# Performance work log

Hardware: AMD Instinct MI355X
Metric: run time of the kernel (lower is better)

Reference implementation:

```python
import jax, jax.numpy as jnp
import numpy as np

W_DIM = 512
NF = 128          # n_features (all blocks equal)
NB = 4            # num_layers / n_blocks
B = 8             # batch
INIT = 32         # initial resolution: 2**(8 - 4 + 1)
IMG = 256         # 2**log_resolution
EPS = 1e-8


def setup_inputs() -> dict:
    key = jax.random.key(0)
    ks = jax.random.split(key, 12)
    d = {}
    d["w"] = jax.random.normal(ks[0], (NB, B, W_DIM), jnp.float32)
    for i in range(NB):
        r = INIT * (2 ** i)
        d[f"noise{i}"] = jax.random.normal(ks[1 + i], (2, B, 1, r, r), jnp.float32)
    # learned parameters
    d["initial_constant"] = jax.random.normal(ks[5], (1, NF, INIT, INIT), jnp.float32)
    d["to_style_w"] = jax.random.normal(ks[6], (NB, NF, W_DIM), jnp.float32)      # EqualizedLinear weights
    d["to_style_b"] = 0.1 * jax.random.normal(ks[7], (NB, NF), jnp.float32)
    d["conv_w"] = jax.random.normal(ks[8], (NB, 2, NF, NF, 3, 3), jnp.float32)    # two StyleBlock convs per block
    d["scale_noise"] = 0.1 * jax.random.normal(ks[9], (NB, 2), jnp.float32)
    d["style_bias"] = 0.1 * jax.random.normal(ks[10], (NB, 2, NF), jnp.float32)
    d["rgb_w"] = jax.random.normal(ks[11], (NB, 1, NF, 1, 1), jnp.float32)        # ToRGB 1x1 convs
    return d


def _resize(x, h, w):
    # bilinear, half-pixel centers (matches F.interpolate align_corners=False)
    return jax.image.resize(x, (x.shape[0], x.shape[1], h, w), "bilinear")


def _mod_conv(x, s, weight, demodulate):
    # x: [B, Cin, H, W], s: [B, Cin], weight: [Cout, Cin, k, k]
    out_c, in_c, k, _ = weight.shape
    c = 1.0 / np.sqrt(in_c * k * k)  # EqualizedWeight scale
    ws = (weight * c)[None] * s[:, None, :, None, None]  # [B, Cout, Cin, k, k]
    if demodulate:
        ws = ws * jax.lax.rsqrt(jnp.sum(ws * ws, axis=(2, 3, 4), keepdims=True) + EPS)
    conv = lambda xi, wi: jax.lax.conv_general_dilated(xi[None], wi, (1, 1), "SAME")[0]
    return jax.vmap(conv)(x, ws)  # per-sample weights == grouped conv with groups=B


def _style_block(x, s, wconv, sn, b, noise):
    x = _mod_conv(x, s, wconv, True)
    x = x + sn * noise
    return jax.nn.leaky_relu(x + b[None, :, None, None], 0.2)


def reference(w, noise0, noise1, noise2, noise3, initial_constant, to_style_w,
              to_style_b, conv_w, scale_noise, style_bias, rgb_w):
    noises = [noise0, noise1, noise2, noise3]
    b = w.shape[1]
    x = jax.nn.relu(jnp.broadcast_to(initial_constant, (b,) + initial_constant.shape[1:]))
    cl = 1.0 / np.sqrt(W_DIM)  # EqualizedLinear scale
    rgb_sum = jnp.zeros((b, 1, IMG, IMG), x.dtype)
    for i in range(NB):
        if i > 0:
            x = _resize(x, x.shape[2] * 2, x.shape[3] * 2)
        s = w[i] @ (to_style_w[i] * cl).T + to_style_b[i]  # [B, NF]
        x = _style_block(x, s, conv_w[i, 0], scale_noise[i, 0], style_bias[i, 0], noises[i][0])
        x = _style_block(x, s, conv_w[i, 1], scale_noise[i, 1], style_bias[i, 1], noises[i][1])
        rgb = _mod_conv(x, s, rgb_w[i], False)  # [B, 1, h, w]
        rgb_sum = rgb_sum + _resize(rgb, IMG, IMG)
    return rgb_sum / 2 + 0.5
```

## Files before the change

### kernel.cpp

```cpp
#include <hip/hip_runtime.h>
#include <math.h>

#define NB 4
#define BATCH 8
#define NF 128
#define WDIM 512
#define EPS_D 1e-8f

typedef unsigned short ushortT;
typedef __attribute__((ext_vector_type(8))) short short8v;
typedef __attribute__((ext_vector_type(8))) unsigned short ushort8v;
typedef __attribute__((ext_vector_type(4))) float float4v;
typedef __attribute__((ext_vector_type(4))) unsigned int uint4v;
typedef __attribute__((ext_vector_type(2))) unsigned int uint2v;

__device__ inline unsigned short f2bf(float f) {
    unsigned u = __builtin_bit_cast(unsigned, f);
    u = (u + 0x7fffu + ((u >> 16) & 1u)) >> 16;
    return (unsigned short)u;
}
__device__ inline float bf2f(unsigned short h) {
    unsigned u = ((unsigned)h) << 16;
    return __builtin_bit_cast(float, u);
}

__global__ void k_style(const float* __restrict__ w,
                        const float* __restrict__ tsw,
                        const float* __restrict__ tsb,
                        float* __restrict__ s) {
    int gid = blockIdx.x * blockDim.x + threadIdx.x;
    if (gid >= NB * BATCH * NF) return;
    int i = gid >> 10;
    int b = (gid >> 7) & 7;
    int o = gid & 127;
    const float cl = 0.044194173824159216f;
    const float* wr = w + (i * BATCH + b) * WDIM;
    const float* tr = tsw + (i * NF + o) * WDIM;
    float acc = 0.f;
    for (int k = 0; k < WDIM; ++k) acc += wr[k] * tr[k];
    s[gid] = acc * cl + tsb[i * NF + o];
}

__global__ void k_demod(const float* __restrict__ conv_w,
                        const float* __restrict__ s,
                        float* __restrict__ d) {
    int bx = blockIdx.x;
    int l = bx >> 7;
    int o = bx & 127;
    int lane = threadIdx.x;
    const float* wb = conv_w + (size_t)((l * NF + o) * NF) * 9;
    float t0 = 0.f, t1 = 0.f;
    for (int k = 0; k < 9; ++k) {
        float a = wb[lane * 9 + k];        t0 += a * a;
        float c = wb[(lane + 64) * 9 + k]; t1 += c * c;
    }
    const float c2 = 1.0f / 1152.0f;
    int i = l >> 1;
    for (int b = 0; b < BATCH; ++b) {
        float s0 = s[(i * BATCH + b) * NF + lane];
        float s1 = s[(i * BATCH + b) * NF + lane + 64];
        float v = t0 * s0 * s0 + t1 * s1 * s1;
        for (int off = 32; off > 0; off >>= 1) v += __shfl_down(v, off);
        if (lane == 0) d[(l * BATCH + b) * NF + o] = rsqrtf(v * c2 + EPS_D);
    }
}

__global__ void k_wmodF(const float* __restrict__ cw, const float* __restrict__ s,
                        ushortT* __restrict__ wm) {
    int idx = blockIdx.x * blockDim.x + threadIdx.x;
    int lane = idx & 63;
    int mf = (idx >> 6) & 7;
    int kcc = (idx >> 9) & 3;
    int t = (idx >> 11) % 9;
    int r2 = idx / (2048 * 9);
    int b = r2 & 7;
    int l = r2 >> 3;
    if (l >= 8) return;
    const float cscale = 0.029462782549439483f;
    int co = mf * 16 + (lane & 15);
    int kb = kcc * 32 + (lane >> 4) * 8;
    const float* src = cw + (((size_t)l * NF + co) * NF) * 9;
    const float* sr = s + ((l >> 1) * BATCH + b) * NF;
    ushort8v o;
    #pragma unroll
    for (int e = 0; e < 8; ++e) {
        int ci = kb + e;
        o[e] = f2bf(src[(size_t)ci * 9 + t] * cscale * sr[ci]);
    }
    *(ushort8v*)(wm + (size_t)idx * 8) = o;
}

__global__ void k_prep_init(const float* __restrict__ ic, ushortT* __restrict__ xp,
                            int total) {
    for (int idx = blockIdx.x * blockDim.x + threadIdx.x; idx < total;
         idx += gridDim.x * blockDim.x) {
        int ci = idx & 127;
        int p = (idx >> 7) & 1023;
        float v = ic[ci * 1024 + p];
        xp[idx] = f2bf(v > 0.f ? v : 0.f);
    }
}

__global__ void k_up2_bf(const ushortT* __restrict__ in, ushortT* __restrict__ out,
                         int h, int w, int total) {
    int W2 = w * 2, H2 = h * 2;
    for (int gid = blockIdx.x * blockDim.x + threadIdx.x; gid < total;
         gid += gridDim.x * blockDim.x) {
        int cg = gid & 15;
        int t = gid >> 4;
        int ox = t % W2; t /= W2;
        int oy = t % H2; int zb = t / H2;
        int y0 = (oy >> 1) - 1 + (oy & 1);
        float wy0 = (oy & 1) ? 0.75f : 0.25f;
        int x0 = (ox >> 1) - 1 + (ox & 1);
        float wx0 = (ox & 1) ? 0.75f : 0.25f;
        int y1 = min(y0 + 1, h - 1); y0 = max(y0, 0);
        int x1 = min(x0 + 1, w - 1); x0 = max(x0, 0);
        const ushortT* base = in + (size_t)zb * h * w * 128 + cg * 8;
        ushort8v v00 = *(const ushort8v*)(base + (size_t)(y0 * w + x0) * 128);
        ushort8v v01 = *(const ushort8v*)(base + (size_t)(y0 * w + x1) * 128);
        ushort8v v10 = *(const ushort8v*)(base + (size_t)(y1 * w + x0) * 128);
        ushort8v v11 = *(const ushort8v*)(base + (size_t)(y1 * w + x1) * 128);
        float wy1 = 1.f - wy0, wx1 = 1.f - wx0;
        ushort8v o;
        #pragma unroll
        for (int k = 0; k < 8; ++k) {
            float v = wy0 * (wx0 * bf2f(v00[k]) + wx1 * bf2f(v01[k]))
                    + wy1 * (wx0 * bf2f(v10[k]) + wx1 * bf2f(v11[k]));
            o[k] = f2bf(v);
        }
        *(ushort8v*)(out + ((size_t)(zb * H2 + oy) * W2 + ox) * 128 + cg * 8) = o;
    }
}

template<int UP2, int NOY>
__global__ __launch_bounds__(256, 3) void k_conv7(
    const ushortT* __restrict__ xp, ushortT* __restrict__ yp,
    const ushortT* __restrict__ wF,
    const float* __restrict__ d_b,
    const float* __restrict__ nz,
    const float* __restrict__ bias,
    const float* __restrict__ sn_ptr,
    const float* __restrict__ s_blk,
    const float* __restrict__ rgbw_i,
    float* __restrict__ rgbb,
    int H, int W, int b0, int do_rgb)
{
    __shared__ __align__(16) char lb[46080];
    int tid = threadIdx.x;
    int lane = tid & 63;
    int wv = tid >> 6;
    int wm = wv & 1;
    int wn = wv >> 1;
    int lm = lane & 15, lk = lane >> 4;
    int tilesX = W >> 4;
    int tx0 = (blockIdx.x % tilesX) << 4;
    int ty0 = (blockIdx.x / tilesX) << 3;
    int zb = blockIdx.y;
    int b = b0 + zb;

    if (!UP2) {
        const char* xbase = (const char*)(xp + (size_t)zb * H * W * 128);
        int offs[6];
        #pragma unroll
        for (int it = 0; it < 6; ++it) {
            int cw = it * 64 + lane;
            int off = -1;
            if (cw < 360) {
                int chunk = wv * 360 + cw;
                int px = chunk >> 3, slot = chunk & 7;
                int hy = px / 18, hx = px - hy * 18;
                int gy = ty0 + hy - 1, gx = tx0 + hx - 1;
                if ((unsigned)gy < (unsigned)H && (unsigned)gx < (unsigned)W)
                    off = (gy * W + gx) * 256 + ((slot ^ (px & 7)) << 4);
            }
            offs[it] = off;
        }
        {
            const uint4v zv = {0, 0, 0, 0};
            #pragma unroll
            for (int c = 0; c < 12; ++c) {
                int idx = tid + c * 256;
                if (idx < 2880) *(uint4v*)(lb + idx * 16) = zv;
            }
        }
        __syncthreads();
        #pragma unroll
        for (int it = 0; it < 6; ++it)
            if (offs[it] >= 0)
                __builtin_amdgcn_global_load_lds(
                    (const __attribute__((address_space(1))) void*)(xbase + offs[it]),
                    (__attribute__((address_space(3))) void*)(lb + wv * 5760 + it * 1024), 16, 0, 0);
        __syncthreads();
        #pragma unroll
        for (int it = 0; it < 6; ++it)
            if (offs[it] >= 0)
                __builtin_amdgcn_global_load_lds(
                    (const __attribute__((address_space(1))) void*)(xbase + offs[it] + 128),
                    (__attribute__((address_space(3))) void*)(lb + 23040 + wv * 5760 + it * 1024), 16, 0, 0);
    } else {
        int h2 = H >> 1, w2 = W >> 1;
        const char* xbase = (const char*)(xp + (size_t)zb * h2 * w2 * 128);
        #pragma unroll
        for (int cih = 0; cih < 2; ++cih) {
            for (int it = 0; it < 6; ++it) {
                int cw = it * 64 + lane;
                if (cw >= 360) break;
                int chunk = wv * 360 + cw;
                int px = chunk >> 3, slot = chunk & 7;
                int hy = px / 18, hx = px - hy * 18;
                int gy = ty0 + hy - 1, gx = tx0 + hx - 1;
                ushort8v o = {0, 0, 0, 0, 0, 0, 0, 0};
                if ((unsigned)gy < (unsigned)H && (unsigned)gx < (unsigned)W) {
                    int sby = ((slot ^ (px & 7)) << 4) + cih * 128;
                    int y0 = (gy >> 1) - 1 + (gy & 1);
                    float wy0 = (gy & 1) ? 0.75f : 0.25f;
                    int x0 = (gx >> 1) - 1 + (gx & 1);
                    float wx0 = (gx & 1) ? 0.75f : 0.25f;
                    int y1 = min(y0 + 1, h2 - 1); y0 = max(y0, 0);
                    int x1 = min(x0 + 1, w2 - 1); x0 = max(x0, 0);
                    ushort8v v00 = *(const ushort8v*)(xbase + (y0 * w2 + x0) * 256 + sby);
                    ushort8v v01 = *(const ushort8v*)(xbase + (y0 * w2 + x1) * 256 + sby);
                    ushort8v v10 = *(const ushort8v*)(xbase + (y1 * w2 + x0) * 256 + sby);
                    ushort8v v11 = *(const ushort8v*)(xbase + (y1 * w2 + x1) * 256 + sby);
                    float wy1 = 1.f - wy0, wx1 = 1.f - wx0;
                    #pragma unroll
                    for (int e = 0; e < 8; ++e) {
                        float v = wy0 * (wx0 * bf2f(v00[e]) + wx1 * bf2f(v01[e]))
                                + wy1 * (wx0 * bf2f(v10[e]) + wx1 * bf2f(v11[e]));
                        o[e] = f2bf(v);
                    }
                }
                *(uint4v*)(lb + cih * 23040 + chunk * 16) = __builtin_bit_cast(uint4v, o);
            }
            if (cih == 0) __syncthreads();
        }
    }

    float4v acc[4][4];
    #pragma unroll
    for (int mf = 0; mf < 4; ++mf)
        #pragma unroll
        for (int nf = 0; nf < 4; ++nf)
            acc[mf][nf] = (float4v){0.f, 0.f, 0.f, 0.f};

    const ushortT* wB = wF + (size_t)b * (9 * 4 * 4096);

    for (int cih = 0; cih < 2; ++cih) {
        if (cih) __syncthreads();
        const char* buf = lb + cih * 23040;
        #pragma unroll
        for (int tap = 0; tap < 9; ++tap) {
            const int dy = (tap < 3) ? 0 : (tap < 6 ? 1 : 2);
            const int dx = tap - dy * 3;
            #pragma unroll
            for (int kc = 0; kc < 2; ++kc) {
                const ushortT* ap = wB + ((size_t)(tap * 4 + cih * 2 + kc) << 12)
                                    + wm * 2048 + lane * 8;
                short8v a0 = *(const short8v*)(ap);
                short8v a1 = *(const short8v*)(ap + 512);
                short8v a2 = *(const short8v*)(ap + 1024);
                short8v a3 = *(const short8v*)(ap + 1536);
                #pragma unroll
                for (int nf = 0; nf < 4; ++nf) {
                    int row = nf * 2 + (lm >> 3) + dy;
                    int col = wn * 8 + (lm & 7) + dx;
                    int hp = row * 18 + col;
                    short8v bf = *(const short8v*)(buf + hp * 128
                                 + ((((kc << 2) + lk) ^ (hp & 7)) << 4));
                    acc[0][nf] = __builtin_amdgcn_mfma_f32_16x16x32_bf16(a0, bf, acc[0][nf], 0, 0, 0);
                    acc[1][nf] = __builtin_amdgcn_mfma_f32_16x16x32_bf16(a1, bf, acc[1][nf], 0, 0, 0);
                    acc[2][nf] = __builtin_amdgcn_mfma_f32_16x16x32_bf16(a2, bf, acc[2][nf], 0, 0, 0);
                    acc[3][nf] = __builtin_amdgcn_mfma_f32_16x16x32_bf16(a3, bf, acc[3][nf], 0, 0, 0);
                }
            }
        }
    }
    __syncthreads();

    float sn = sn_ptr[0];
    float nv[4];
    #pragma unroll
    for (int nf = 0; nf < 4; ++nf) {
        int gy = ty0 + nf * 2 + (lm >> 3);
        int gx = tx0 + wn * 8 + (lm & 7);
        nv[nf] = sn * nz[((size_t)b * H + gy) * W + gx];
    }
    const float cl2 = 0.08838834764831845f;

    if (NOY) {
        float rgbs[4] = {0.f, 0.f, 0.f, 0.f};
        #pragma unroll
        for (int mf = 0; mf < 4; ++mf) {
            int co0 = wm * 64 + mf * 16 + lk * 4;
            float4v dd = *(const float4v*)(d_b + b * 128 + co0);
            float4v bb = *(const float4v*)(bias + co0);
            float4v rw = *(const float4v*)(rgbw_i + co0);
            float4v sv = *(const float4v*)(s_blk + b * 128 + co0);
            #pragma unroll
            for (int nf = 0; nf < 4; ++nf) {
                #pragma unroll
                for (int e = 0; e < 4; ++e) {
                    float t = acc[mf][nf][e] * dd[e] + nv[nf] + bb[e];
                    t = t > 0.f ? t : 0.2f * t;
                    rgbs[nf] += t * rw[e] * cl2 * sv[e];
                }
            }
        }
        #pragma unroll
        for (int nf = 0; nf < 4; ++nf) {
            float r = rgbs[nf];
            r += __shfl_xor(r, 16, 64);
            r += __shfl_xor(r, 32, 64);
            if (lane < 16) {
                int gy = ty0 + nf * 2 + (lane >> 3);
                int gx = tx0 + wn * 8 + (lane & 7);
                rgbb[((size_t)(wm * BATCH + b) * H + gy) * W + gx] = r;
            }
        }
        return;
    }

    float rgbs[4] = {0.f, 0.f, 0.f, 0.f};
    unsigned pka[4][4][2];
    #pragma unroll
    for (int mf = 0; mf < 4; ++mf) {
        int co0 = wm * 64 + mf * 16 + lk * 4;
        float4v dd = *(const float4v*)(d_b + b * 128 + co0);
        float4v bb = *(const float4v*)(bias + co0);
        float4v cf = {0.f, 0.f, 0.f, 0.f};
        if (do_rgb) {
            float4v rw = *(const float4v*)(rgbw_i + co0);
            float4v sv = *(const float4v*)(s_blk + b * 128 + co0);
            #pragma unroll
            for (int e = 0; e < 4; ++e) cf[e] = rw[e] * cl2 * sv[e];
        }
        #pragma unroll
        for (int nf = 0; nf < 4; ++nf) {
            float v[4];
            #pragma unroll
            for (int e = 0; e < 4; ++e) {
                float t = acc[mf][nf][e] * dd[e] + nv[nf] + bb[e];
                v[e] = t > 0.f ? t : 0.2f * t;
            }
            if (do_rgb)
                rgbs[nf] += v[0] * cf[0] + v[1] * cf[1] + v[2] * cf[2] + v[3] * cf[3];
            pka[mf][nf][0] = (unsigned)f2bf(v[0]) | ((unsigned)f2bf(v[1]) << 16);
            pka[mf][nf][1] = (unsigned)f2bf(v[2]) | ((unsigned)f2bf(v[3]) << 16);
        }
    }
    if (do_rgb) {
        #pragma unroll
        for (int nf = 0; nf < 4; ++nf) {
            float r = rgbs[nf];
            r += __shfl_xor(r, 16, 64);
            r += __shfl_xor(r, 32, 64);
            if (lane < 16) {
                int gy = ty0 + nf * 2 + (lane >> 3);
                int gx = tx0 + wn * 8 + (lane & 7);
                rgbb[((size_t)(wm * BATCH + b) * H + gy) * W + gx] = r;
            }
        }
    }
    char* xb2 = (char*)(yp + (size_t)zb * H * W * 128);
    #pragma unroll
    for (int h = 0; h < 2; ++h) {
        if (wm == h) {
            #pragma unroll
            for (int mf = 0; mf < 4; ++mf) {
                int cb = (mf * 16 + lk * 4) * 2;
                #pragma unroll
                for (int nf = 0; nf < 4; ++nf) {
                    int pxl = (nf * 2 + (lm >> 3)) * 16 + wn * 8 + (lm & 7);
                    int ad = pxl * 128 + (cb ^ ((pxl & 7) << 4));
                    uint2v pk2;
                    pk2[0] = pka[mf][nf][0];
                    pk2[1] = pka[mf][nf][1];
                    *(uint2v*)(lb + ad) = pk2;
                }
            }
        }
        __syncthreads();
        for (int c = tid; c < 1024; c += 256) {
            int pxl = c >> 3, ck = c & 7;
            uint4v v = *(const uint4v*)(lb + pxl * 128 + ((ck << 4) ^ ((pxl & 7) << 4)));
            int gy = ty0 + (pxl >> 4), gx = tx0 + (pxl & 15);
            *(uint4v*)(xb2 + ((size_t)(gy * W + gx)) * 256 + h * 128 + ck * 16) = v;
        }
        if (h == 0) __syncthreads();
    }
}

__global__ void k_rgbacc(const float* __restrict__ rgb, float* __restrict__ acc,
                         int r, int beta, int b0, int g) {
    int idx = blockIdx.x * blockDim.x + threadIdx.x;
    if (idx >= g * 256 * 256) return;
    int ox = idx & 255;
    int oy = (idx >> 8) & 255;
    int b = b0 + (idx >> 16);
    float scale = (float)r * (1.0f / 256.0f);
    float fy = (oy + 0.5f) * scale - 0.5f;
    float fx = (ox + 0.5f) * scale - 0.5f;
    int y0 = (int)floorf(fy); float wy = fy - (float)y0;
    int x0 = (int)floorf(fx); float wx = fx - (float)x0;
    int y1 = min(y0 + 1, r - 1); y0 = max(y0, 0);
    int x1 = min(x0 + 1, r - 1); x0 = max(x0, 0);
    const float* p0 = rgb + (size_t)b * r * r;
    const float* p1 = rgb + (size_t)(BATCH + b) * r * r;
    float v00 = p0[y0 * r + x0] + p1[y0 * r + x0];
    float v01 = p0[y0 * r + x1] + p1[y0 * r + x1];
    float v10 = p0[y1 * r + x0] + p1[y1 * r + x0];
    float v11 = p0[y1 * r + x1] + p1[y1 * r + x1];
    float v = (1.f - wy) * ((1.f - wx) * v00 + wx * v01)
            +        wy  * ((1.f - wx) * v10 + wx * v11);
    int oidx = (b << 16) | (oy << 8) | ox;
    acc[oidx] = (beta ? acc[oidx] : 0.f) + v;
}

__global__ void k_final(float* __restrict__ out, int total) {
    int idx = blockIdx.x * blockDim.x + threadIdx.x;
    if (idx < total) out[idx] = out[idx] * 0.5f + 0.5f;
}

extern "C" void kernel_launch(void* const* d_in, const int* in_sizes, int n_in,
                              void* d_out, int out_size, void* d_ws, size_t ws_size,
                              hipStream_t stream) {
    const float* w     = (const float*)d_in[0];
    const float* noise[4] = {(const float*)d_in[1], (const float*)d_in[2],
                             (const float*)d_in[3], (const float*)d_in[4]};
    const float* ic    = (const float*)d_in[5];
    const float* tsw   = (const float*)d_in[6];
    const float* tsb   = (const float*)d_in[7];
    const float* cw    = (const float*)d_in[8];
    const float* snp   = (const float*)d_in[9];
    const float* sbias = (const float*)d_in[10];
    const float* rgbw  = (const float*)d_in[11];

    const size_t WM_BYTES = 8ull * 8 * 9 * 4 * 8 * 64 * 8 * 2;
    const size_t RGBB = 2ull * BATCH * 65536 * 4;
    const size_t FIXED = 16384 + 32768 + RGBB + WM_BYTES;
    const size_t PER_S = 65536ull * 128 * 2;
    int g = 0;
    for (int cand = 8; cand >= 1; cand >>= 1)
        if (ws_size >= FIXED + 2ull * cand * PER_S) { g = cand; break; }
    if (g == 0) return;

    char* ws = (char*)d_ws;
    float* s_all   = (float*)ws;
    float* d_all   = (float*)(ws + 16384);
    float* rgbb    = (float*)(ws + 49152);
    ushortT* wmall = (ushortT*)(ws + 49152 + RGBB);
    ushortT* bufA  = (ushortT*)(ws + FIXED);
    ushortT* bufB  = (ushortT*)(ws + FIXED + (size_t)g * PER_S);
    float* accb    = (float*)d_out;

    k_style<<<64, 64, 0, stream>>>(w, tsw, tsb, s_all);
    k_demod<<<1024, 64, 0, stream>>>(cw, s_all, d_all);
    k_wmodF<<<4608, 256, 0, stream>>>(cw, s_all, wmall);

    #define CONV(T1, T2, SRC, DST, L, R, B0, G, RGB) do {                      \
        dim3 grid(((R) / 16) * ((R) / 8), (G));                                \
        k_conv7<T1, T2><<<grid, 256, 0, stream>>>((SRC), (DST),                \
            wmall + (size_t)(L) * (8 * 9 * 4 * 4096), d_all + (L) * BATCH * NF,\
            noise[(L) >> 1] + (size_t)((L) & 1) * BATCH * (R) * (R),           \
            sbias + (L) * NF, snp + (L), s_all + ((L) >> 1) * BATCH * NF,      \
            rgbw + ((L) >> 1) * NF, rgbb, (R), (R), (B0), (RGB));              \
    } while (0)

    if (g >= 2) {
        ushortT* xb = bufA;
        ushortT* tb = bufB;
        k_prep_init<<<4096, 256, 0, stream>>>(ic, xb, BATCH * 1024 * 128);
        for (int i = 0; i < 3; ++i) {
            int r = 32 << i;
            if (i > 0) {
                int total = BATCH * r * r * 16;
                int blocks = (total + 255) / 256;
                if (blocks > 2048) blocks = 2048;
                k_up2_bf<<<blocks, 256, 0, stream>>>(xb, tb, r / 2, r / 2, total);
                ushortT* t2 = xb; xb = tb; tb = t2;
            }
            CONV(0, 0, xb, tb, i * 2 + 0, r, 0, BATCH, 0);
            { ushortT* t2 = xb; xb = tb; tb = t2; }
            CONV(0, 0, xb, tb, i * 2 + 1, r, 0, BATCH, 1);
            { ushortT* t2 = xb; xb = tb; tb = t2; }
            int tot = BATCH * 256 * 256;
            k_rgbacc<<<(tot + 255) / 256, 256, 0, stream>>>(rgbb, accb, r, i > 0, 0, BATCH);
        }
        ushortT* x128 = xb;
        ushortT* big  = tb;
        for (int b0 = 0; b0 < BATCH; b0 += g) {
            CONV(1, 0, x128 + (size_t)b0 * 2097152, big, 6, 256, b0, g, 0);
            CONV(0, 1, big, big, 7, 256, b0, g, 1);
            int tot = g * 256 * 256;
            k_rgbacc<<<(tot + 255) / 256, 256, 0, stream>>>(rgbb, accb, 256, 1, b0, g);
        }
    } else {
        for (int b0 = 0; b0 < BATCH; ++b0) {
            ushortT* xb = bufA;
            ushortT* tb = bufB;
            k_prep_init<<<1024, 256, 0, stream>>>(ic, xb, 1024 * 128);
            for (int i = 0; i < NB; ++i) {
                int r = 32 << i;
                if (i > 0) {
                    int total = r * r * 16;
                    int blocks = (total + 255) / 256;
                    if (blocks > 2048) blocks = 2048;
                    k_up2_bf<<<blocks, 256, 0, stream>>>(xb, tb, r / 2, r / 2, total);
                    ushortT* t2 = xb; xb = tb; tb = t2;
                }
                CONV(0, 0, xb, tb, i * 2 + 0, r, b0, 1, 0);
                { ushortT* t2 = xb; xb = tb; tb = t2; }
                if (i < 3) {
                    CONV(0, 0, xb, tb, i * 2 + 1, r, b0, 1, 1);
                    { ushortT* t2 = xb; xb = tb; tb = t2; }
                } else {
                    CONV(0, 1, xb, tb, 7, r, b0, 1, 1);
                }
                int tot = 1 * 256 * 256;
                k_rgbacc<<<(tot + 255) / 256, 256, 0, stream>>>(rgbb, accb, r, i > 0, b0, 1);
            }
        }
    }
    #undef CONV
    k_final<<<(out_size + 255) / 256, 256, 0, stream>>>(accb, out_size);
}
```

Before: 826.0 us.

## Fuse upsample and both 256-res style convs plus RGB into one kernel

Adds k_mega, which for each 16x8 output tile upsamples the 128x128 input on the fly, computes the first conv over an 18x10 halo region into shared memory, then runs the second conv and the ToRGB reduction directly from that LDS intermediate. This replaces the batched loop of two k_conv7 launches that wrote and re-read the full 256x256x128 intermediate through global memory. The cost is recomputing the first conv on halo pixels (180 versus 128 positions), more LDS per block with lower occupancy (launch bounds of 2), and more accumulator registers. The now-unused UP2 path is removed from k_conv7.

Result: no change. 837.9 us (+1.4%).

```diff
diff --git a/kernel.cpp b/kernel.cpp
--- a/kernel.cpp
+++ b/kernel.cpp
@@ -133,25 +133,20 @@
     }
 }
 
-template<int UP2, int NOY>
+template<int NOY>
 __global__ __launch_bounds__(256, 3) void k_conv7(
     const ushortT* __restrict__ xp, ushortT* __restrict__ yp,
-    const ushortT* __restrict__ wF,
-    const float* __restrict__ d_b,
-    const float* __restrict__ nz,
-    const float* __restrict__ bias,
-    const float* __restrict__ sn_ptr,
-    const float* __restrict__ s_blk,
-    const float* __restrict__ rgbw_i,
-    float* __restrict__ rgbb,
+    const ushortT* __restrict__ wF, const float* __restrict__ d_b,
+    const float* __restrict__ nz, const float* __restrict__ bias,
+    const float* __restrict__ sn_ptr, const float* __restrict__ s_blk,
+    const float* __restrict__ rgbw_i, float* __restrict__ rgbb,
     int H, int W, int b0, int do_rgb)
 {
     __shared__ __align__(16) char lb[46080];
     int tid = threadIdx.x;
     int lane = tid & 63;
     int wv = tid >> 6;
-    int wm = wv & 1;
-    int wn = wv >> 1;
+    int wm = wv & 1, wn = wv >> 1;
     int lm = lane & 15, lk = lane >> 4;
     int tilesX = W >> 4;
     int tx0 = (blockIdx.x % tilesX) << 4;
@@ -159,83 +154,44 @@
     int zb = blockIdx.y;
     int b = b0 + zb;
 
-    if (!UP2) {
-        const char* xbase = (const char*)(xp + (size_t)zb * H * W * 128);
-        int offs[6];
-        #pragma unroll
-        for (int it = 0; it < 6; ++it) {
-            int cw = it * 64 + lane;
-            int off = -1;
-            if (cw < 360) {
-                int chunk = wv * 360 + cw;
-                int px = chunk >> 3, slot = chunk & 7;
-                int hy = px / 18, hx = px - hy * 18;
-                int gy = ty0 + hy - 1, gx = tx0 + hx - 1;
-                if ((unsigned)gy < (unsigned)H && (unsigned)gx < (unsigned)W)
-                    off = (gy * W + gx) * 256 + ((slot ^ (px & 7)) << 4);
-            }
-            offs[it] = off;
-        }
-        {
-            const uint4v zv = {0, 0, 0, 0};
-            #pragma unroll
-            for (int c = 0; c < 12; ++c) {
-                int idx = tid + c * 256;
-                if (idx < 2880) *(uint4v*)(lb + idx * 16) = zv;
-            }
-        }
-        __syncthreads();
-        #pragma unroll
-        for (int it = 0; it < 6; ++it)
-            if (offs[it] >= 0)
-                __builtin_amdgcn_global_load_lds(
-                    (const __attribute__((address_space(1))) void*)(xbase + offs[it]),
-                    (__attribute__((address_space(3))) void*)(lb + wv * 5760 + it * 1024), 16, 0, 0);
-        __syncthreads();
-        #pragma unroll
-        for (int it = 0; it < 6; ++it)
-            if (offs[it] >= 0)
-                __builtin_amdgcn_global_load_lds(
-                    (const __attribute__((address_space(1))) void*)(xbase + offs[it] + 128),
-                    (__attribute__((address_space(3))) void*)(lb + 23040 + wv * 5760 + it * 1024), 16, 0, 0);
-    } else {
-        int h2 = H >> 1, w2 = W >> 1;
-        const char* xbase = (const char*)(xp + (size_t)zb * h2 * w2 * 128);
-        #pragma unroll
-        for (int cih = 0; cih < 2; ++cih) {
-            for (int it = 0; it < 6; ++it) {
-                int cw = it * 64 + lane;
-                if (cw >= 360) break;
-                int chunk = wv * 360 + cw;
-                int px = chunk >> 3, slot = chunk & 7;
-                int hy = px / 18, hx = px - hy * 18;
-                int gy = ty0 + hy - 1, gx = tx0 + hx - 1;
-                ushort8v o = {0, 0, 0, 0, 0, 0, 0, 0};
-                if ((unsigned)gy < (unsigned)H && (unsigned)gx < (unsigned)W) {
-                    int sby = ((slot ^ (px & 7)) << 4) + cih * 128;
-                    int y0 = (gy >> 1) - 1 + (gy & 1);
-                    float wy0 = (gy & 1) ? 0.75f : 0.25f;
-                    int x0 = (gx >> 1) - 1 + (gx & 1);
-                    float wx0 = (gx & 1) ? 0.75f : 0.25f;
-                    int y1 = min(y0 + 1, h2 - 1); y0 = max(y0, 0);
-                    int x1 = min(x0 + 1, w2 - 1); x0 = max(x0, 0);
-                    ushort8v v00 = *(const ushort8v*)(xbase + (y0 * w2 + x0) * 256 + sby);
-                    ushort8v v01 = *(const ushort8v*)(xbase + (y0 * w2 + x1) * 256 + sby);
-                    ushort8v v10 = *(const ushort8v*)(xbase + (y1 * w2 + x0) * 256 + sby);
-                    ushort8v v11 = *(const ushort8v*)(xbase + (y1 * w2 + x1) * 256 + sby);
-                    float wy1 = 1.f - wy0, wx1 = 1.f - wx0;
-                    #pragma unroll
-                    for (int e = 0; e < 8; ++e) {
-                        float v = wy0 * (wx0 * bf2f(v00[e]) + wx1 * bf2f(v01[e]))
-                                + wy1 * (wx0 * bf2f(v10[e]) + wx1 * bf2f(v11[e]));
-                        o[e] = f2bf(v);
-                    }
-                }
-                *(uint4v*)(lb + cih * 23040 + chunk * 16) = __builtin_bit_cast(uint4v, o);
-            }
-            if (cih == 0) __syncthreads();
-        }
-    }
+    const char* xbase = (const char*)(xp + (size_t)zb * H * W * 128);
+    int offs[6];
+    #pragma unroll
+    for (int it = 0; it < 6; ++it) {
+        int cw = it * 64 + lane;
+        int off = -1;
+        if (cw < 360) {
+            int chunk = wv * 360 + cw;
+            int px = chunk >> 3, slot = chunk & 7;
+            int hy = px / 18, hx = px - hy * 18;
+            int gy = ty0 + hy - 1, gx = tx0 + hx - 1;
+            if ((unsigned)gy < (unsigned)H && (unsigned)gx < (unsigned)W)
+                off = (gy * W + gx) * 256 + ((slot ^ (px & 7)) << 4);
+        }
+        offs[it] = off;
+    }
+    {
+        const uint4v zv = {0, 0, 0, 0};
+        #pragma unroll
+        for (int c = 0; c < 12; ++c) {
+            int idx = tid + c * 256;
+            if (idx < 2880) *(uint4v*)(lb + idx * 16) = zv;
+        }
+    }
+    __syncthreads();
+    #pragma unroll
+    for (int it = 0; it < 6; ++it)
+        if (offs[it] >= 0)
+            __builtin_amdgcn_global_load_lds(
+                (const __attribute__((address_space(1))) void*)(xbase + offs[it]),
+                (__attribute__((address_space(3))) void*)(lb + wv * 5760 + it * 1024), 16, 0, 0);
+    __syncthreads();
+    #pragma unroll
+    for (int it = 0; it < 6; ++it)
+        if (offs[it] >= 0)
+            __builtin_amdgcn_global_load_lds(
+                (const __attribute__((address_space(1))) void*)(xbase + offs[it] + 128),
+                (__attribute__((address_space(3))) void*)(lb + 23040 + wv * 5760 + it * 1024), 16, 0, 0);
 
     float4v acc[4][4];
     #pragma unroll
@@ -245,7 +201,6 @@
             acc[mf][nf] = (float4v){0.f, 0.f, 0.f, 0.f};
 
     const ushortT* wB = wF + (size_t)b * (9 * 4 * 4096);
-
     for (int cih = 0; cih < 2; ++cih) {
         if (cih) __syncthreads();
         const char* buf = lb + cih * 23040;
@@ -298,14 +253,13 @@
             float4v rw = *(const float4v*)(rgbw_i + co0);
             float4v sv = *(const float4v*)(s_blk + b * 128 + co0);
             #pragma unroll
-            for (int nf = 0; nf < 4; ++nf) {
+            for (int nf = 0; nf < 4; ++nf)
                 #pragma unroll
                 for (int e = 0; e < 4; ++e) {
                     float t = acc[mf][nf][e] * dd[e] + nv[nf] + bb[e];
                     t = t > 0.f ? t : 0.2f * t;
                     rgbs[nf] += t * rw[e] * cl2 * sv[e];
                 }
-            }
         }
         #pragma unroll
         for (int nf = 0; nf < 4; ++nf) {
@@ -388,6 +342,210 @@
             *(uint4v*)(xb2 + ((size_t)(gy * W + gx)) * 256 + h * 128 + ck * 16) = v;
         }
         if (h == 0) __syncthreads();
+    }
+}
+
+__global__ __launch_bounds__(256, 2) void k_mega(
+    const ushortT* __restrict__ x128,
+    const ushortT* __restrict__ wm6,
+    const ushortT* __restrict__ wm7,
+    const float* __restrict__ d6, const float* __restrict__ d7,
+    const float* __restrict__ nz6, const float* __restrict__ nz7,
+    const float* __restrict__ bias6, const float* __restrict__ bias7,
+    const float* __restrict__ sn6p, const float* __restrict__ sn7p,
+    const float* __restrict__ s_blk, const float* __restrict__ rgbw_i,
+    float* __restrict__ rgbb)
+{
+    __shared__ __align__(16) char lb[61440];
+    const int J0 = 15360;
+    int tid = threadIdx.x;
+    int lane = tid & 63;
+    int wv = tid >> 6;
+    int wm = wv & 1, wn = wv >> 1;
+    int lm = lane & 15, lk = lane >> 4;
+    int tx0 = (blockIdx.x & 15) << 4;
+    int ty0 = (blockIdx.x >> 4) << 3;
+    int b = blockIdx.y;
+
+    int ib[6], prr[6], pcc[6];
+    bool pv[6];
+    #pragma unroll
+    for (int nf = 0; nf < 6; ++nf) {
+        int p = wn * 96 + nf * 16 + lm;
+        pv[nf] = (p < 180);
+        int pc = pv[nf] ? p : 0;
+        prr[nf] = pc / 18;
+        pcc[nf] = pc - prr[nf] * 18;
+        ib[nf] = prr[nf] * 20 + pcc[nf];
+    }
+
+    float4v j0a[4][6];
+    #pragma unroll
+    for (int mf = 0; mf < 4; ++mf)
+        #pragma unroll
+        for (int nf = 0; nf < 6; ++nf)
+            j0a[mf][nf] = (float4v){0.f, 0.f, 0.f, 0.f};
+
+    const ushortT* wB6 = wm6 + (size_t)b * (9 * 4 * 4096);
+    const ushortT* wB7 = wm7 + (size_t)b * (9 * 4 * 4096);
+    const char* xbase = (const char*)(x128 + (size_t)b * 128 * 128 * 128);
+
+    for (int q = 0; q < 4; ++q) {
+        #pragma unroll
+        for (int k = 0; k < 4; ++k) {
+            int c = tid + k * 256;
+            if (c < 960) {
+                int ip = c >> 2, s = c & 3;
+                int iy = ip / 20, ix = ip - iy * 20;
+                int oy = ty0 + iy - 2, ox = tx0 + ix - 2;
+                ushort8v o = {0, 0, 0, 0, 0, 0, 0, 0};
+                if ((unsigned)oy < 256u && (unsigned)ox < 256u) {
+                    int sby = q * 64 + s * 16;
+                    int y0 = (oy >> 1) - 1 + (oy & 1);
+                    float wy0 = (oy & 1) ? 0.75f : 0.25f;
+                    int x0 = (ox >> 1) - 1 + (ox & 1);
+                    float wx0 = (ox & 1) ? 0.75f : 0.25f;
+                    int y1 = min(y0 + 1, 127); y0 = max(y0, 0);
+                    int x1 = min(x0 + 1, 127); x0 = max(x0, 0);
+                    ushort8v v00 = *(const ushort8v*)(xbase + (y0 * 128 + x0) * 256 + sby);
+                    ushort8v v01 = *(const ushort8v*)(xbase + (y0 * 128 + x1) * 256 + sby);
+                    ushort8v v10 = *(const ushort8v*)(xbase + (y1 * 128 + x0) * 256 + sby);
+                    ushort8v v11 = *(const ushort8v*)(xbase + (y1 * 128 + x1) * 256 + sby);
+                    float wy1 = 1.f - wy0, wx1 = 1.f - wx0;
+                    #pragma unroll
+                    for (int e = 0; e < 8; ++e) {
+                        float v = wy0 * (wx0 * bf2f(v00[e]) + wx1 * bf2f(v01[e]))
+                                + wy1 * (wx0 * bf2f(v10[e]) + wx1 * bf2f(v11[e]));
+                        o[e] = f2bf(v);
+                    }
+                }
+                *(uint4v*)(lb + ip * 64 + ((s ^ (ip & 3)) << 4)) = __builtin_bit_cast(uint4v, o);
+            }
+        }
+        __syncthreads();
+        #pragma unroll
+        for (int tap = 0; tap < 9; ++tap) {
+            const int dy = (tap < 3) ? 0 : (tap < 6 ? 1 : 2);
+            const int dx = tap - dy * 3;
+            const ushortT* ap = wB6 + ((size_t)(tap * 4 + q) << 12) + wm * 2048 + lane * 8;
+            short8v a0 = *(const short8v*)(ap);
+            short8v a1 = *(const short8v*)(ap + 512);
+            short8v a2 = *(const short8v*)(ap + 1024);
+            short8v a3 = *(const short8v*)(ap + 1536);
+            #pragma unroll
+            for (int nf = 0; nf < 6; ++nf) {
+                int ipx = ib[nf] + dy * 20 + dx;
+                short8v bf = *(const short8v*)(lb + ipx * 64 + ((lk ^ (ipx & 3)) << 4));
+                j0a[0][nf] = __builtin_amdgcn_mfma_f32_16x16x32_bf16(a0, bf, j0a[0][nf], 0, 0, 0);
+                j0a[1][nf] = __builtin_amdgcn_mfma_f32_16x16x32_bf16(a1, bf, j0a[1][nf], 0, 0, 0);
+                j0a[2][nf] = __builtin_amdgcn_mfma_f32_16x16x32_bf16(a2, bf, j0a[2][nf], 0, 0, 0);
+                j0a[3][nf] = __builtin_amdgcn_mfma_f32_16x16x32_bf16(a3, bf, j0a[3][nf], 0, 0, 0);
+            }
+        }
+        __syncthreads();
+    }
+
+    {
+        float sn6 = sn6p[0];
+        #pragma unroll
+        for (int nf = 0; nf < 6; ++nf) {
+            if (!pv[nf]) continue;
+            int p = wn * 96 + nf * 16 + lm;
+            int oy = ty0 + prr[nf] - 1, ox = tx0 + pcc[nf] - 1;
+            bool inimg = ((unsigned)oy < 256u) && ((unsigned)ox < 256u);
+            float nv = inimg ? sn6 * nz6[((size_t)b * 256 + oy) * 256 + ox] : 0.f;
+            #pragma unroll
+            for (int mf = 0; mf < 4; ++mf) {
+                int co0 = wm * 64 + mf * 16 + lk * 4;
+                uint2v pk2 = {0u, 0u};
+                if (inimg) {
+                    float4v dd = *(const float4v*)(d6 + b * 128 + co0);
+                    float4v bb = *(const float4v*)(bias6 + co0);
+                    float v[4];
+                    #pragma unroll
+                    for (int e = 0; e < 4; ++e) {
+                        float t = j0a[mf][nf][e] * dd[e] + nv + bb[e];
+                        v[e] = t > 0.f ? t : 0.2f * t;
+                    }
+                    pk2[0] = (unsigned)f2bf(v[0]) | ((unsigned)f2bf(v[1]) << 16);
+                    pk2[1] = (unsigned)f2bf(v[2]) | ((unsigned)f2bf(v[3]) << 16);
+                }
+                int ad = p * 256 + ((co0 * 2) ^ ((p & 7) << 4));
+                *(uint2v*)(lb + J0 + ad) = pk2;
+            }
+        }
+    }
+    __syncthreads();
+
+    float4v acc[4][4];
+    #pragma unroll
+    for (int mf = 0; mf < 4; ++mf)
+        #pragma unroll
+        for (int nf = 0; nf < 4; ++nf)
+            acc[mf][nf] = (float4v){0.f, 0.f, 0.f, 0.f};
+
+    #pragma unroll
+    for (int tap = 0; tap < 9; ++tap) {
+        const int dy = (tap < 3) ? 0 : (tap < 6 ? 1 : 2);
+        const int dx = tap - dy * 3;
+        #pragma unroll
+        for (int kcc = 0; kcc < 4; ++kcc) {
+            const ushortT* ap = wB7 + ((size_t)(tap * 4 + kcc) << 12) + wm * 2048 + lane * 8;
+            short8v a0 = *(const short8v*)(ap);
+            short8v a1 = *(const short8v*)(ap + 512);
+            short8v a2 = *(const short8v*)(ap + 1024);
+            short8v a3 = *(const short8v*)(ap + 1536);
+            #pragma unroll
+            for (int nf = 0; nf < 4; ++nf) {
+                int row = nf * 2 + (lm >> 3) + dy;
+                int col = wn * 8 + (lm & 7) + dx;
+                int hp = row * 18 + col;
+                short8v bf = *(const short8v*)(lb + J0 + hp * 256
+                             + ((kcc * 64 + lk * 16) ^ ((hp & 7) << 4)));
+                acc[0][nf] = __builtin_amdgcn_mfma_f32_16x16x32_bf16(a0, bf, acc[0][nf], 0, 0, 0);
+                acc[1][nf] = __builtin_amdgcn_mfma_f32_16x16x32_bf16(a1, bf, acc[1][nf], 0, 0, 0);
+                acc[2][nf] = __builtin_amdgcn_mfma_f32_16x16x32_bf16(a2, bf, acc[2][nf], 0, 0, 0);
+                acc[3][nf] = __builtin_amdgcn_mfma_f32_16x16x32_bf16(a3, bf, acc[3][nf], 0, 0, 0);
+            }
+        }
+    }
+
+    float sn7 = sn7p[0];
+    float nv7[4];
+    #pragma unroll
+    for (int nf = 0; nf < 4; ++nf) {
+        int gy = ty0 + nf * 2 + (lm >> 3);
+        int gx = tx0 + wn * 8 + (lm & 7);
+        nv7[nf] = sn7 * nz7[((size_t)b * 256 + gy) * 256 + gx];
+    }
+    const float cl2 = 0.08838834764831845f;
+    float rgbs[4] = {0.f, 0.f, 0.f, 0.f};
+    #pragma unroll
+    for (int mf = 0; mf < 4; ++mf) {
+        int co0 = wm * 64 + mf * 16 + lk * 4;
+        float4v dd = *(const float4v*)(d7 + b * 128 + co0);
+        float4v bb = *(const float4v*)(bias7 + co0);
+        float4v rw = *(const float4v*)(rgbw_i + co0);
+        float4v sv = *(const float4v*)(s_blk + b * 128 + co0);
+        #pragma unroll
+        for (int nf = 0; nf < 4; ++nf)
+            #pragma unroll
+            for (int e = 0; e < 4; ++e) {
+                float t = acc[mf][nf][e] * dd[e] + nv7[nf] + bb[e];
+                t = t > 0.f ? t : 0.2f * t;
+                rgbs[nf] += t * rw[e] * cl2 * sv[e];
+            }
+    }
+    #pragma unroll
+    for (int nf = 0; nf < 4; ++nf) {
+        float r = rgbs[nf];
+        r += __shfl_xor(r, 16, 64);
+        r += __shfl_xor(r, 32, 64);
+        if (lane < 16) {
+            int gy = ty0 + nf * 2 + (lane >> 3);
+            int gx = tx0 + wn * 8 + (lane & 7);
+            rgbb[((size_t)(wm * BATCH + b) * 256 + gy) * 256 + gx] = r;
+        }
     }
 }
 
@@ -458,9 +616,9 @@
     k_demod<<<1024, 64, 0, stream>>>(cw, s_all, d_all);
     k_wmodF<<<4608, 256, 0, stream>>>(cw, s_all, wmall);
 
-    #define CONV(T1, T2, SRC, DST, L, R, B0, G, RGB) do {                      \
+    #define CONV(T2, SRC, DST, L, R, B0, G, RGB) do {                          \
         dim3 grid(((R) / 16) * ((R) / 8), (G));                                \
-        k_conv7<T1, T2><<<grid, 256, 0, stream>>>((SRC), (DST),                \
+        k_conv7<T2><<<grid, 256, 0, stream>>>((SRC), (DST),                    \
             wmall + (size_t)(L) * (8 * 9 * 4 * 4096), d_all + (L) * BATCH * NF,\
             noise[(L) >> 1] + (size_t)((L) & 1) * BATCH * (R) * (R),           \
             sbias + (L) * NF, snp + (L), s_all + ((L) >> 1) * BATCH * NF,      \
@@ -480,21 +638,22 @@
                 k_up2_bf<<<blocks, 256, 0, stream>>>(xb, tb, r / 2, r / 2, total);
                 ushortT* t2 = xb; xb = tb; tb = t2;
             }
-            CONV(0, 0, xb, tb, i * 2 + 0, r, 0, BATCH, 0);
+            CONV(0, xb, tb, i * 2 + 0, r, 0, BATCH, 0);
             { ushortT* t2 = xb; xb = tb; tb = t2; }
-            CONV(0, 0, xb, tb, i * 2 + 1, r, 0, BATCH, 1);
+            CONV(0, xb, tb, i * 2 + 1, r, 0, BATCH, 1);
             { ushortT* t2 = xb; xb = tb; tb = t2; }
             int tot = BATCH * 256 * 256;
             k_rgbacc<<<(tot + 255) / 256, 256, 0, stream>>>(rgbb, accb, r, i > 0, 0, BATCH);
         }
-        ushortT* x128 = xb;
-        ushortT* big  = tb;
-        for (int b0 = 0; b0 < BATCH; b0 += g) {
-            CONV(1, 0, x128 + (size_t)b0 * 2097152, big, 6, 256, b0, g, 0);
-            CONV(0, 1, big, big, 7, 256, b0, g, 1);
-            int tot = g * 256 * 256;
-            k_rgbacc<<<(tot + 255) / 256, 256, 0, stream>>>(rgbb, accb, 256, 1, b0, g);
-        }
+        dim3 mgrid(512, BATCH);
+        k_mega<<<mgrid, 256, 0, stream>>>(xb,
+            wmall + 6ull * (8 * 9 * 4 * 4096), wmall + 7ull * (8 * 9 * 4 * 4096),
+            d_all + 6 * BATCH * NF, d_all + 7 * BATCH * NF,
+            noise[3], noise[3] + (size_t)BATCH * 65536,
+            sbias + 6 * NF, sbias + 7 * NF, snp + 6, snp + 7,
+            s_all + 3 * BATCH * NF, rgbw + 3 * NF, rgbb);
+        int tot = BATCH * 256 * 256;
+        k_rgbacc<<<(tot + 255) / 256, 256, 0, stream>>>(rgbb, accb, 256, 1, 0, BATCH);
     } else {
         for (int b0 = 0; b0 < BATCH; ++b0) {
             ushortT* xb = bufA;
@@ -509,13 +668,13 @@
                     k_up2_bf<<<blocks, 256, 0, stream>>>(xb, tb, r / 2, r / 2, total);
                     ushortT* t2 = xb; xb = tb; tb = t2;
                 }
-                CONV(0, 0, xb, tb, i * 2 + 0, r, b0, 1, 0);
+                CONV(0, xb, tb, i * 2 + 0, r, b0, 1, 0);
                 { ushortT* t2 = xb; xb = tb; tb = t2; }
                 if (i < 3) {
-                    CONV(0, 0, xb, tb, i * 2 + 1, r, b0, 1, 1);
+                    CONV(0, xb, tb, i * 2 + 1, r, b0, 1, 1);
                     { ushortT* t2 = xb; xb = tb; tb = t2; }
                 } else {
-                    CONV(0, 1, xb, tb, 7, r, b0, 1, 1);
+                    CONV(1, xb, tb, 7, r, b0, 1, 1);
                 }
                 int tot = 1 * 256 * 256;
                 k_rgbacc<<<(tot + 255) / 256, 256, 0, stream>>>(rgbb, accb, r, i > 0, b0, 1);
```
